# Optimization experiments

Hardware: AMD Instinct MI355X
Metric: run time of the kernel (lower is better)

Reference implementation:

```python
import jax, jax.numpy as jnp
import numpy as np

OUT_F, IN_F = 4096, 11008
NUMEL = OUT_F * IN_F            # divisible by 256
NUM_SUPER = NUMEL // 256        # super-blocks of 8 sub-blocks x 32 values


def setup_inputs() -> dict:
    key = jax.random.key(0)
    k = jax.random.split(key, 7)
    x = jax.random.normal(k[0], (64, IN_F), dtype=jnp.float32)
    packed = jax.random.randint(k[1], (NUMEL // 2,), 0, 256, dtype=jnp.int32)
    d = jax.random.uniform(k[2], (NUM_SUPER,), dtype=jnp.float32) * 0.02
    dmin = jax.random.uniform(k[3], (NUM_SUPER,), dtype=jnp.float32) * 0.02
    scales = jax.random.randint(k[4], (NUM_SUPER * 8,), 0, 64, dtype=jnp.int32)
    mins = jax.random.randint(k[5], (NUM_SUPER * 8,), 0, 64, dtype=jnp.int32)
    bias = jax.random.normal(k[6], (OUT_F,), dtype=jnp.float32) * 0.02
    return {"x": x, "packed": packed, "d": d, "dmin": dmin,
            "scales": scales, "mins": mins, "bias": bias}


def _dequant_q4k(packed, d, dmin, scales, mins):
    # unpack two 4-bit quants per byte, interleaved low/high (stack dim=1 + flatten)
    low = packed & 15
    high = (packed >> 4) & 15
    q = jnp.stack([low, high], axis=1).reshape(NUM_SUPER, 8, 32).astype(jnp.float32)
    sc = (scales.astype(jnp.float32) / 63.0).reshape(NUM_SUPER, 8, 1)
    mn = (mins.astype(jnp.float32) / 63.0).reshape(NUM_SUPER, 8, 1)
    normalized = q / 15.0 * sc + mn
    w = normalized * d.reshape(NUM_SUPER, 1, 1) + dmin.reshape(NUM_SUPER, 1, 1)
    return w.reshape(OUT_F, IN_F)


def reference(x, packed, d, dmin, scales, mins, bias):
    w = _dequant_q4k(packed, d, dmin, scales, mins)   # [OUT_F, IN_F] fp32
    return x @ w.T + bias                              # F.linear
```

## Files before the change

### kernel.cpp

```cpp
#include <hip/hip_runtime.h>
#include <stdint.h>

#define OUT_F   4096
#define IN_F    11008
#define BATCH   64
#define NSUP    43
#define SB_ROW  344
#define IPR     5504
#define NKS     8
#define XP_BYTES   (4 * 344 * 64 * 16)
#define PART_ELEMS ((size_t)NKS * BATCH * OUT_F)
#define WS_FULL    (XP_BYTES + PART_ELEMS * 4)

typedef __attribute__((ext_vector_type(8))) short  short8;
typedef __attribute__((ext_vector_type(4))) float  floatx4;
typedef __attribute__((ext_vector_type(4))) int    intx4;

template<int N> struct IC { static constexpr int value = N; };

__device__ __forceinline__ unsigned pack_bf16(float f0, float f1) {
    return __builtin_amdgcn_perm(__float_as_uint(f1), __float_as_uint(f0), 0x07060302u);
}

__device__ __forceinline__ void glds16(const void* g, void* s) {
    __builtin_amdgcn_global_load_lds(
        (const __attribute__((address_space(1))) uint32_t*)g,
        (__attribute__((address_space(3))) uint32_t*)s,
        16, 0, 0);
}

__device__ __forceinline__ void group_fence(void) {
    asm volatile("" ::: "memory");
    __builtin_amdgcn_sched_barrier(0);
}

__global__ __launch_bounds__(256) void xprep_kernel(const float* __restrict__ x,
                                                    intx4* __restrict__ xp) {
    const int ksb = blockIdx.x;
    const int mt  = threadIdx.x >> 6;
    const int l   = threadIdx.x & 63;
    const int lo  = l & 15, hi = l >> 4;
    const float* src = x + (mt * 16 + lo) * IN_F + ksb * 32 + hi * 8;
    floatx4 a0 = *(const floatx4*)src;
    floatx4 a1 = *(const floatx4*)(src + 4);
    intx4 r;
    r.x = pack_bf16(a0.x, a0.y);
    r.y = pack_bf16(a0.z, a0.w);
    r.z = pack_bf16(a1.x, a1.y);
    r.w = pack_bf16(a1.z, a1.w);
    xp[(mt * 344 + ksb) * 64 + l] = r;
}

__global__ __launch_bounds__(256) void init_out_kernel(const float* __restrict__ bias,
                                                       float* __restrict__ out) {
    int i = blockIdx.x * 256 + threadIdx.x;
    out[i] = bias[i & (OUT_F - 1)];
}

__global__ __launch_bounds__(256) void reduce_kernel(const float* __restrict__ part,
                                                     const float* __restrict__ bias,
                                                     float* __restrict__ out) {
    const int i = blockIdx.x * 256 + threadIdx.x;
    float s = bias[i & (OUT_F - 1)];
    #pragma unroll
    for (int k = 0; k < NKS; ++k) s += part[(size_t)k * (BATCH * OUT_F) + i];
    out[i] = s;
}

template<bool USE_PART>
__global__ __launch_bounds__(256, 2) void qlin_main(
    const intx4* __restrict__ xp,
    const int*   __restrict__ packed,
    const float* __restrict__ dd,
    const float* __restrict__ dmn_g,
    const int*   __restrict__ scales,
    const int*   __restrict__ mins,
    float*       __restrict__ part,
    float*       __restrict__ out)
{
    __shared__ intx4 xfs[2][2048];

    const int nb  = blockIdx.x & 63;
    const int ks  = blockIdx.x >> 6;
    const int tid = threadIdx.x;
    const int w   = tid >> 6;
    const int l   = tid & 63;
    const int lo  = l & 15, hi = l >> 4;
    const int wq  = tid & 192;

    const int o    = nb * 64 + w * 16 + lo;
    const int sup0 = ks < 3 ? 6 * ks : 18 + 5 * (ks - 3);
    const int nsup = ks < 3 ? 6 : 5;

    floatx4 acc[4];
    #pragma unroll
    for (int mt = 0; mt < 4; ++mt) acc[mt] = (floatx4)0.0f;

    const int*   bp0 = packed + o * IPR + sup0 * 128 + hi * 4;
    const int*   scp = scales + o * SB_ROW + sup0 * 8;
    const int*   mnp = mins   + o * SB_ROW + sup0 * 8;
    const float* dp  = dd     + o * NSUP + sup0;
    const float* dmp = dmn_g  + o * NSUP + sup0;

    auto stage_x = [&](int sup_abs, int buf) {
        #pragma unroll
        for (int i = 0; i < 8; ++i) {
            const intx4* src = xp + (i >> 1) * 22016 + sup_abs * 512 + (i & 1) * 256 + tid;
            glds16((const void*)src, (void*)&xfs[buf][i * 256 + wq]);
        }
    };

    auto run = [&](auto nsc) {
        constexpr int NS = decltype(nsc)::value;
        intx4 br[NS][8];
        intx4 s0[NS], s1[NS], m0[NS], m1[NS];
        float dv[NS], dmv[NS];

        auto issue_w = [&](int s) {
            #pragma unroll
            for (int st = 0; st < 8; ++st)
                br[s][st] = __builtin_nontemporal_load((const intx4*)(bp0 + s * 128 + st * 16));
            s0[s]  = *(const intx4*)(scp + s * 8);
            s1[s]  = *(const intx4*)(scp + s * 8 + 4);
            m0[s]  = *(const intx4*)(mnp + s * 8);
            m1[s]  = *(const intx4*)(mnp + s * 8 + 4);
            dv[s]  = dp[s];
            dmv[s] = dmp[s];
        };

        auto compute_sup = [&](int s, int buf) {
            const float A945 = dv[s] * (1.0f / 945.0f);
            const float A63  = dv[s] * (1.0f / 63.0f);
            #pragma unroll
            for (int st = 0; st < 8; ++st) {
                const int scv = (st < 4) ? s0[s][st & 3] : s1[s][st & 3];
                const int mnv = (st < 4) ? m0[s][st & 3] : m1[s][st & 3];
                const float A = A945 * (float)scv;
                const float B = fmaf(A63, (float)mnv, dmv[s]);
                const int v0 = br[s][st].x, v1 = br[s][st].y;
                const int v2 = br[s][st].z, v3 = br[s][st].w;
                union { intx4 i; short8 s8; } uw;
                uw.i.x = pack_bf16(fmaf((float)(v0 & 15), A, B), fmaf((float)(v0 >> 4), A, B));
                uw.i.y = pack_bf16(fmaf((float)(v1 & 15), A, B), fmaf((float)(v1 >> 4), A, B));
                uw.i.z = pack_bf16(fmaf((float)(v2 & 15), A, B), fmaf((float)(v2 >> 4), A, B));
                uw.i.w = pack_bf16(fmaf((float)(v3 & 15), A, B), fmaf((float)(v3 >> 4), A, B));

                union { intx4 i; short8 s8; } u0, u1, u2, u3;
                u0.i = xfs[buf][0 * 512 + st * 64 + l];
                u1.i = xfs[buf][1 * 512 + st * 64 + l];
                u2.i = xfs[buf][2 * 512 + st * 64 + l];
                u3.i = xfs[buf][3 * 512 + st * 64 + l];
                acc[0] = __builtin_amdgcn_mfma_f32_16x16x32_bf16(u0.s8, uw.s8, acc[0], 0, 0, 0);
                acc[1] = __builtin_amdgcn_mfma_f32_16x16x32_bf16(u1.s8, uw.s8, acc[1], 0, 0, 0);
                acc[2] = __builtin_amdgcn_mfma_f32_16x16x32_bf16(u2.s8, uw.s8, acc[2], 0, 0, 0);
                acc[3] = __builtin_amdgcn_mfma_f32_16x16x32_bf16(u3.s8, uw.s8, acc[3], 0, 0, 0);
            }
        };

        issue_w(0); stage_x(sup0 + 0, 0);
        group_fence();
        issue_w(1); stage_x(sup0 + 1, 1);
        group_fence();

        #pragma unroll
        for (int s = 0; s < NS; ++s) {
            if (s + 1 < NS) asm volatile("s_waitcnt vmcnt(22)" ::: "memory");
            else            asm volatile("s_waitcnt vmcnt(0)"  ::: "memory");
            __builtin_amdgcn_sched_barrier(0);
            __builtin_amdgcn_s_barrier();

            if (s + 2 < NS) issue_w(s + 2);

            compute_sup(s, s & 1);

            if (s + 2 < NS) {
                __builtin_amdgcn_s_barrier();
                stage_x(sup0 + s + 2, s & 1);
                group_fence();
            }
        }
    };
    if (nsup == 6) run(IC<6>{});
    else           run(IC<5>{});

    if (USE_PART) {
        float* pbase = part + (size_t)ks * (BATCH * OUT_F) + o;
        #pragma unroll
        for (int mt = 0; mt < 4; ++mt) {
            #pragma unroll
            for (int rr = 0; rr < 4; ++rr)
                pbase[(mt * 16 + hi * 4 + rr) * OUT_F] = acc[mt][rr];
        }
    } else {
        #pragma unroll
        for (int mt = 0; mt < 4; ++mt) {
            #pragma unroll
            for (int rr = 0; rr < 4; ++rr)
                atomicAdd(out + (mt * 16 + hi * 4 + rr) * OUT_F + o, acc[mt][rr]);
        }
    }
}

extern "C" void kernel_launch(void* const* d_in, const int* in_sizes, int n_in,
                              void* d_out, int out_size, void* d_ws, size_t ws_size,
                              hipStream_t stream) {
    (void)in_sizes; (void)n_in; (void)out_size;
    const float* x      = (const float*)d_in[0];
    const int*   packed = (const int*)d_in[1];
    const float* d      = (const float*)d_in[2];
    const float* dmin   = (const float*)d_in[3];
    const int*   scales = (const int*)d_in[4];
    const int*   mins   = (const int*)d_in[5];
    const float* bias   = (const float*)d_in[6];
    float* out = (float*)d_out;

    const bool has_part = ws_size >= (size_t)WS_FULL;
    intx4* xp   = (intx4*)d_ws;
    float* part = (float*)((char*)d_ws + XP_BYTES);

    xprep_kernel<<<344, 256, 0, stream>>>(x, xp);

    if (has_part) {
        qlin_main<true><<<64 * NKS, 256, 0, stream>>>(
            xp, packed, d, dmin, scales, mins, part, out);
        reduce_kernel<<<(BATCH * OUT_F) / 256, 256, 0, stream>>>(part, bias, out);
    } else {
        init_out_kernel<<<(BATCH * OUT_F) / 256, 256, 0, stream>>>(bias, out);
        qlin_main<false><<<64 * NKS, 256, 0, stream>>>(
            xp, packed, d, dmin, scales, mins, part, out);
    }
}
```

Baseline: 166.1 us.

## Stage packed weights through LDS with XOR swizzle and half-superblock pipeline

Weight nibbles were loaded straight into registers (a two-superblock register prefetch). They are now copied into LDS with direct global-to-LDS loads and an XOR swizzle so that each wave's LDS reads avoid bank conflicts. The pipeline is restructured into half-superblock steps with double buffering, and each buffer is restaged after a barrier. This cuts register pressure and should raise occupancy, but it adds more barriers and LDS traffic and gives a shallower prefetch depth.

```diff
diff --git a/kernel.cpp b/kernel.cpp
--- a/kernel.cpp
+++ b/kernel.cpp
@@ -78,17 +78,18 @@
     float*       __restrict__ part,
     float*       __restrict__ out)
 {
-    __shared__ intx4 xfs[2][2048];
+    __shared__ intx4 xl[2][1024];
+    __shared__ intx4 wl[2][1024];
 
     const int nb  = blockIdx.x & 63;
     const int ks  = blockIdx.x >> 6;
     const int tid = threadIdx.x;
-    const int w   = tid >> 6;
+    const int wv  = tid >> 6;
     const int l   = tid & 63;
     const int lo  = l & 15, hi = l >> 4;
-    const int wq  = tid & 192;
-
-    const int o    = nb * 64 + w * 16 + lo;
+    const int lo7 = lo & 7;
+
+    const int o    = nb * 64 + wv * 16 + lo;
     const int sup0 = ks < 3 ? 6 * ks : 18 + 5 * (ks - 3);
     const int nsup = ks < 3 ? 6 : 5;
 
@@ -96,87 +97,102 @@
     #pragma unroll
     for (int mt = 0; mt < 4; ++mt) acc[mt] = (floatx4)0.0f;
 
-    const int*   bp0 = packed + o * IPR + sup0 * 128 + hi * 4;
     const int*   scp = scales + o * SB_ROW + sup0 * 8;
     const int*   mnp = mins   + o * SB_ROW + sup0 * 8;
     const float* dp  = dd     + o * NSUP + sup0;
     const float* dmp = dmn_g  + o * NSUP + sup0;
 
-    auto stage_x = [&](int sup_abs, int buf) {
-        #pragma unroll
-        for (int i = 0; i < 8; ++i) {
-            const intx4* src = xp + (i >> 1) * 22016 + sup_abs * 512 + (i & 1) * 256 + tid;
-            glds16((const void*)src, (void*)&xfs[buf][i * 256 + wq]);
+    auto stage = [&](int sup, int par, int b) {
+        #pragma unroll
+        for (int j = 0; j < 4; ++j) {
+            const int row  = j * 4 + hi;
+            const int usrc = (l & 15) ^ (row & 7);
+            const int* gw = packed + (size_t)(nb * 64 + wv * 16 + row) * IPR
+                            + sup * 128 + par * 64 + usrc * 4;
+            glds16((const void*)gw, (void*)&wl[b][wv * 256 + j * 64]);
+        }
+        #pragma unroll
+        for (int j = 0; j < 4; ++j) {
+            const intx4* gx = xp + (wv * 344 + sup * 8 + par * 4 + j) * 64 + l;
+            glds16((const void*)gx, (void*)&xl[b][(wv * 4 + j) * 64]);
+        }
+    };
+
+    auto compute_half = [&](int b, intx4 sv, intx4 mv, float dvv, float dmvv) {
+        const float A945 = dvv * (1.0f / 945.0f);
+        const float A63  = dvv * (1.0f / 63.0f);
+        const int wbase  = wv * 256 + lo * 16;
+        #pragma unroll
+        for (int st2 = 0; st2 < 4; ++st2) {
+            const float A = A945 * (float)sv[st2];
+            const float B = fmaf(A63, (float)mv[st2], dmvv);
+            const intx4 wr = wl[b][wbase + (((st2 * 4 + hi) ^ lo7))];
+            const int v0 = wr.x, v1 = wr.y, v2 = wr.z, v3 = wr.w;
+            union { intx4 i; short8 s8; } uw;
+            uw.i.x = pack_bf16(fmaf((float)(v0 & 15), A, B), fmaf((float)(v0 >> 4), A, B));
+            uw.i.y = pack_bf16(fmaf((float)(v1 & 15), A, B), fmaf((float)(v1 >> 4), A, B));
+            uw.i.z = pack_bf16(fmaf((float)(v2 & 15), A, B), fmaf((float)(v2 >> 4), A, B));
+            uw.i.w = pack_bf16(fmaf((float)(v3 & 15), A, B), fmaf((float)(v3 >> 4), A, B));
+
+            union { intx4 i; short8 s8; } u0, u1, u2, u3;
+            u0.i = xl[b][(0 * 4 + st2) * 64 + l];
+            u1.i = xl[b][(1 * 4 + st2) * 64 + l];
+            u2.i = xl[b][(2 * 4 + st2) * 64 + l];
+            u3.i = xl[b][(3 * 4 + st2) * 64 + l];
+            acc[0] = __builtin_amdgcn_mfma_f32_16x16x32_bf16(u0.s8, uw.s8, acc[0], 0, 0, 0);
+            acc[1] = __builtin_amdgcn_mfma_f32_16x16x32_bf16(u1.s8, uw.s8, acc[1], 0, 0, 0);
+            acc[2] = __builtin_amdgcn_mfma_f32_16x16x32_bf16(u2.s8, uw.s8, acc[2], 0, 0, 0);
+            acc[3] = __builtin_amdgcn_mfma_f32_16x16x32_bf16(u3.s8, uw.s8, acc[3], 0, 0, 0);
         }
     };
 
     auto run = [&](auto nsc) {
         constexpr int NS = decltype(nsc)::value;
-        intx4 br[NS][8];
-        intx4 s0[NS], s1[NS], m0[NS], m1[NS];
-        float dv[NS], dmv[NS];
-
-        auto issue_w = [&](int s) {
-            #pragma unroll
-            for (int st = 0; st < 8; ++st)
-                br[s][st] = __builtin_nontemporal_load((const intx4*)(bp0 + s * 128 + st * 16));
-            s0[s]  = *(const intx4*)(scp + s * 8);
-            s1[s]  = *(const intx4*)(scp + s * 8 + 4);
-            m0[s]  = *(const intx4*)(mnp + s * 8);
-            m1[s]  = *(const intx4*)(mnp + s * 8 + 4);
-            dv[s]  = dp[s];
-            dmv[s] = dmp[s];
-        };
-
-        auto compute_sup = [&](int s, int buf) {
-            const float A945 = dv[s] * (1.0f / 945.0f);
-            const float A63  = dv[s] * (1.0f / 63.0f);
-            #pragma unroll
-            for (int st = 0; st < 8; ++st) {
-                const int scv = (st < 4) ? s0[s][st & 3] : s1[s][st & 3];
-                const int mnv = (st < 4) ? m0[s][st & 3] : m1[s][st & 3];
-                const float A = A945 * (float)scv;
-                const float B = fmaf(A63, (float)mnv, dmv[s]);
-                const int v0 = br[s][st].x, v1 = br[s][st].y;
-                const int v2 = br[s][st].z, v3 = br[s][st].w;
-                union { intx4 i; short8 s8; } uw;
-                uw.i.x = pack_bf16(fmaf((float)(v0 & 15), A, B), fmaf((float)(v0 >> 4), A, B));
-                uw.i.y = pack_bf16(fmaf((float)(v1 & 15), A, B), fmaf((float)(v1 >> 4), A, B));
-                uw.i.z = pack_bf16(fmaf((float)(v2 & 15), A, B), fmaf((float)(v2 >> 4), A, B));
-                uw.i.w = pack_bf16(fmaf((float)(v3 & 15), A, B), fmaf((float)(v3 >> 4), A, B));
-
-                union { intx4 i; short8 s8; } u0, u1, u2, u3;
-                u0.i = xfs[buf][0 * 512 + st * 64 + l];
-                u1.i = xfs[buf][1 * 512 + st * 64 + l];
-                u2.i = xfs[buf][2 * 512 + st * 64 + l];
-                u3.i = xfs[buf][3 * 512 + st * 64 + l];
-                acc[0] = __builtin_amdgcn_mfma_f32_16x16x32_bf16(u0.s8, uw.s8, acc[0], 0, 0, 0);
-                acc[1] = __builtin_amdgcn_mfma_f32_16x16x32_bf16(u1.s8, uw.s8, acc[1], 0, 0, 0);
-                acc[2] = __builtin_amdgcn_mfma_f32_16x16x32_bf16(u2.s8, uw.s8, acc[2], 0, 0, 0);
-                acc[3] = __builtin_amdgcn_mfma_f32_16x16x32_bf16(u3.s8, uw.s8, acc[3], 0, 0, 0);
+        intx4 cs0, cm0, cs1, cm1;  float cdv, cdmv;
+        intx4 ns0, nm0, ns1, nm1;  float ndv, ndmv;
+
+        cs0  = *(const intx4*)(scp);
+        cm0  = *(const intx4*)(mnp);
+        cdv  = dp[0];
+        cdmv = dmp[0];
+        stage(sup0, 0, 0);
+        group_fence();
+        cs1  = *(const intx4*)(scp + 4);
+        cm1  = *(const intx4*)(mnp + 4);
+        stage(sup0, 1, 1);
+        group_fence();
+
+        #pragma unroll
+        for (int s = 0; s < NS; ++s) {
+            const int sup = sup0 + s;
+            asm volatile("s_waitcnt vmcnt(10)" ::: "memory");
+            __builtin_amdgcn_sched_barrier(0);
+            __builtin_amdgcn_s_barrier();
+            compute_half(0, cs0, cm0, cdv, cdmv);
+            __builtin_amdgcn_sched_barrier(0);
+            __builtin_amdgcn_s_barrier();
+            if (s + 1 < NS) {
+                ns0  = *(const intx4*)(scp + (s + 1) * 8);
+                nm0  = *(const intx4*)(mnp + (s + 1) * 8);
+                ndv  = dp[s + 1];
+                ndmv = dmp[s + 1];
+                stage(sup + 1, 0, 0);
             }
-        };
-
-        issue_w(0); stage_x(sup0 + 0, 0);
-        group_fence();
-        issue_w(1); stage_x(sup0 + 1, 1);
-        group_fence();
-
-        #pragma unroll
-        for (int s = 0; s < NS; ++s) {
-            if (s + 1 < NS) asm volatile("s_waitcnt vmcnt(22)" ::: "memory");
-            else            asm volatile("s_waitcnt vmcnt(0)"  ::: "memory");
-            __builtin_amdgcn_sched_barrier(0);
-            __builtin_amdgcn_s_barrier();
-
-            if (s + 2 < NS) issue_w(s + 2);
-
-            compute_sup(s, s & 1);
-
-            if (s + 2 < NS) {
-                __builtin_amdgcn_s_barrier();
-                stage_x(sup0 + s + 2, s & 1);
+            group_fence();
+            if (s + 1 < NS) { asm volatile("s_waitcnt vmcnt(12)" ::: "memory"); }
+            else            { asm volatile("s_waitcnt vmcnt(0)"  ::: "memory"); }
+            __builtin_amdgcn_sched_barrier(0);
+            __builtin_amdgcn_s_barrier();
+            compute_half(1, cs1, cm1, cdv, cdmv);
+            __builtin_amdgcn_sched_barrier(0);
+            __builtin_amdgcn_s_barrier();
+            if (s + 1 < NS) {
+                ns1 = *(const intx4*)(scp + (s + 1) * 8 + 4);
+                nm1 = *(const intx4*)(mnp + (s + 1) * 8 + 4);
+                stage(sup + 1, 1, 1);
                 group_fence();
+                cs0 = ns0; cm0 = nm0; cdv = ndv; cdmv = ndmv;
+                cs1 = ns1; cm1 = nm1;
             }
         }
     };
```

Result: slower. 171.0 us (+3.0%).
